# Kernel tuning notes

Measured on AMD Instinct MI355X. Metric: run time of the kernel, lower is better.

## Reference

```python
import jax, jax.numpy as jnp
import numpy as np

B, S, D, H, DK, F = 4, 2048, 1024, 16, 64, 4096


def layer_norm(x, g, b, eps=1e-5):
    mu = jnp.mean(x, axis=-1, keepdims=True)
    var = jnp.var(x, axis=-1, keepdims=True)
    return (x - mu) * jax.lax.rsqrt(var + eps) * g + b


def setup_inputs() -> dict:
    key = jax.random.key(0)
    ks = jax.random.split(key, 16)
    s = 0.02
    return {
        "src": jax.random.normal(ks[0], (B, S, D), jnp.float32),
        # per-head q/k/v projections stacked over heads: (H, D, DK)
        "Wq": jax.random.normal(ks[1], (H, D, DK), jnp.float32) * s,
        "bq": jnp.zeros((H, DK), jnp.float32),
        "Wk": jax.random.normal(ks[2], (H, D, DK), jnp.float32) * s,
        "bk": jnp.zeros((H, DK), jnp.float32),
        "Wv": jax.random.normal(ks[3], (H, D, DK), jnp.float32) * s,
        "bv": jnp.zeros((H, DK), jnp.float32),
        "Wo": jax.random.normal(ks[4], (H * DK, D), jnp.float32) * s,
        "bo": jnp.zeros((D,), jnp.float32),
        "ln1_g": jnp.ones((D,), jnp.float32),
        "ln1_b": jnp.zeros((D,), jnp.float32),
        "W1": jax.random.normal(ks[5], (D, F), jnp.float32) * s,
        "b1": jnp.zeros((F,), jnp.float32),
        "W2": jax.random.normal(ks[6], (F, D), jnp.float32) * s,
        "b2": jnp.zeros((D,), jnp.float32),
        "ln2_g": jnp.ones((D,), jnp.float32),
        "ln2_b": jnp.zeros((D,), jnp.float32),
    }


def reference(src, Wq, bq, Wk, bk, Wv, bv, Wo, bo, ln1_g, ln1_b, W1, b1, W2, b2, ln2_g, ln2_b):
    # --- multi-head attention (all heads batched via einsum) ---
    q = jnp.einsum("bsd,hdk->bhsk", src, Wq) + bq[None, :, None, :]
    k = jnp.einsum("bsd,hdk->bhsk", src, Wk) + bk[None, :, None, :]
    v = jnp.einsum("bsd,hdk->bhsk", src, Wv) + bv[None, :, None, :]
    scale = jnp.sqrt(jnp.asarray(DK, q.dtype))
    scores = jnp.einsum("bhqk,bhsk->bhqs", q, k) / scale  # [B,H,S,S]
    p = jax.nn.softmax(scores, axis=-1)
    ctx = jnp.einsum("bhqs,bhsk->bhqk", p, v)             # [B,H,S,DK]
    ctx = ctx.transpose(0, 2, 1, 3).reshape(src.shape[0], src.shape[1], H * DK)
    attn_out = ctx @ Wo + bo
    x = layer_norm(src + attn_out, ln1_g, ln1_b)
    # --- feed-forward ---
    ff = jax.nn.relu(x @ W1 + b1) @ W2 + b2
    return layer_norm(x + ff, ln2_g, ln2_b)
```

## Files before the change

kernel.cpp:

```cpp
#include <hip/hip_runtime.h>
#include <hip/hip_bf16.h>
#include <cstddef>
#include <cstdint>

typedef __bf16 bf16;
typedef __bf16 bf16x4 __attribute__((ext_vector_type(4)));
typedef __bf16 bf16x8 __attribute__((ext_vector_type(8)));
typedef float f32x4 __attribute__((ext_vector_type(4)));
typedef float f32x16 __attribute__((ext_vector_type(16)));
typedef unsigned int u32x4 __attribute__((ext_vector_type(4)));

#define GLD_LDS16(g, l) __builtin_amdgcn_global_load_lds( \
    (const __attribute__((address_space(1))) void*)(g),   \
    (__attribute__((address_space(3))) void*)(l), 16, 0, 0)

#define SBAR __builtin_amdgcn_s_barrier()
#define SCHED0 __builtin_amdgcn_sched_barrier(0)

static __device__ inline unsigned int cvtpk(float lo, float hi) {
  unsigned int r;
  asm("v_cvt_pk_bf16_f32 %0, %1, %2" : "=v"(r) : "v"(lo), "v"(hi));
  return r;
}
static __device__ inline void plswap(unsigned int& a, unsigned int& b) {
  asm("v_permlane32_swap_b32 %0, %1" : "+v"(a), "+v"(b));
}
static __device__ inline float fexp2(float x) {
#if __has_builtin(__builtin_amdgcn_exp2f)
  return __builtin_amdgcn_exp2f(x);
#else
  float r; asm("v_exp_f32 %0, %1" : "=v"(r) : "v"(x)); return r;
#endif
}
static __device__ inline float tsum16(const float* e) {
  float s0 = e[0] + e[1], s1 = e[2] + e[3], s2 = e[4] + e[5], s3 = e[6] + e[7];
  float s4 = e[8] + e[9], s5 = e[10] + e[11], s6 = e[12] + e[13], s7 = e[14] + e[15];
  return ((s0 + s1) + (s2 + s3)) + ((s4 + s5) + (s6 + s7));
}

__global__ void __launch_bounds__(256)
k_cast(const float* __restrict__ in, bf16* __restrict__ out) {
  int gid = blockIdx.x * 256 + threadIdx.x;
  f32x4 a = ((const f32x4*)in)[gid * 2];
  f32x4 b = ((const f32x4*)in)[gid * 2 + 1];
  bf16x8 o;
#pragma unroll
  for (int i = 0; i < 4; ++i) { o[i] = (bf16)a[i]; o[i + 4] = (bf16)b[i]; }
  ((bf16x8*)out)[gid] = o;
}

__global__ void __launch_bounds__(256)
k_transpose_t(const float* __restrict__ in, bf16* __restrict__ out, int R, int C) {
  __shared__ float tile[64][68];
  const int nct = C >> 6;
  const int bc = blockIdx.x % nct, br = blockIdx.x / nct;
  const int r0 = br << 6, c0 = bc << 6;
  const int t = threadIdx.x;
  const int tr = t >> 4, tc4 = (t & 15) << 2;
#pragma unroll
  for (int i = 0; i < 4; ++i)
    *(f32x4*)&tile[i * 16 + tr][tc4] =
        *(const f32x4*)&in[(size_t)(r0 + i * 16 + tr) * C + c0 + tc4];
  __syncthreads();
  const int c = t >> 2, rch = (t & 3) << 4;
  bf16 ob[16];
#pragma unroll
  for (int j = 0; j < 16; ++j) ob[j] = (bf16)tile[rch + j][c];
  bf16* dst = out + (size_t)(c0 + c) * R + r0 + rch;
  *(bf16x8*)&dst[0] = *(bf16x8*)&ob[0];
  *(bf16x8*)&dst[8] = *(bf16x8*)&ob[8];
}

__global__ void __launch_bounds__(256)
k_reorder_qkv_t(const float* __restrict__ Wq, const float* __restrict__ Wk,
                const float* __restrict__ Wv, bf16* __restrict__ WqkvT) {
  __shared__ float tile[64][68];
  const int bid = blockIdx.x;
  const int sub = bid >> 4, tl = bid & 15;
  const int proj = sub >> 4, h = sub & 15;
  const float* W = (proj == 0) ? Wq : (proj == 1) ? Wk : Wv;
  const float* src = W + (size_t)h * 65536;
  const int r0 = tl << 6;
  const int t = threadIdx.x, tr = t >> 4, tc4 = (t & 15) << 2;
#pragma unroll
  for (int i = 0; i < 4; ++i)
    *(f32x4*)&tile[i * 16 + tr][tc4] =
        *(const f32x4*)&src[(size_t)(r0 + i * 16 + tr) * 64 + tc4];
  __syncthreads();
  const int c = t >> 2, rch = (t & 3) << 4;
  bf16 ob[16];
#pragma unroll
  for (int j = 0; j < 16; ++j) ob[j] = (bf16)tile[rch + j][c];
  bf16* dst = WqkvT + ((size_t)(proj * 1024 + h * 64 + c)) * 1024 + r0 + rch;
  *(bf16x8*)&dst[0] = *(bf16x8*)&ob[0];
  *(bf16x8*)&dst[8] = *(bf16x8*)&ob[8];
}

__global__ void __launch_bounds__(256)
k_bias_qkv(const float* __restrict__ bq, const float* __restrict__ bk,
           const float* __restrict__ bv, float* __restrict__ bqkv) {
  int n = blockIdx.x * 256 + threadIdx.x;
  int proj = n >> 10, wi = n & 1023;
  const float* bb = (proj == 0) ? bq : (proj == 1) ? bk : bv;
  bqkv[n] = bb[wi];
}

template <int MODE, int NREP>
__global__ void __launch_bounds__(512, 1)
k_gemm8(const bf16* __restrict__ A, const bf16* __restrict__ Bt,
        const float* __restrict__ bias, void* __restrict__ outp,
        int M, int N, int K,
        bf16* __restrict__ qb, bf16* __restrict__ kb, bf16* __restrict__ vb) {
  constexpr int BN = 128 * NREP;
  constexpr int BROWS = 64 * NREP;
  __shared__ __align__(16) bf16 Asl[4][8192];
  __shared__ __align__(16) bf16 Bsl[4][BROWS * 64];

  const int tid = threadIdx.x;
  const int lane = tid & 63, wave = tid >> 6;
  const int l16 = lane & 15, lq = lane >> 4;
  const int qwm = wave >> 2, qwn = wave & 3;

  const int mtiles = M >> 8;
  const int nwg = gridDim.x, cpx = nwg >> 3;
  const int wg = (blockIdx.x & 7) * cpx + (blockIdx.x >> 3);
  const int tile_m = (wg % mtiles) << 8;
  const int tile_n = (wg / mtiles) * BN;

  const bf16* Abase = A + (size_t)tile_m * K;
  const bf16* Bbase = Bt + (size_t)tile_n * K;

  const int crow = tid >> 3;
  const int ccol = ((tid & 7) ^ (crow & 7)) << 3;

  auto stageA = [&](int T, int h, int slot) {
    const bf16* s_ = Abase + (size_t)(h * 128 + crow) * K + T * 64 + ccol;
    GLD_LDS16(s_, &Asl[slot][tid * 8]);
    GLD_LDS16(s_ + (size_t)64 * K, &Asl[slot][tid * 8 + 4096]);
  };
  auto stageB = [&](int T, int h, int slot) {
    const bf16* s_ = Bbase + (size_t)(h * BROWS + crow) * K + T * 64 + ccol;
    GLD_LDS16(s_, &Bsl[slot][tid * 8]);
    if (NREP == 2) GLD_LDS16(s_ + (size_t)64 * K, &Bsl[slot][tid * 8 + 4096]);
  };

  const int xk = l16 & 7;
  const int swz0 = (lq ^ xk) * 16;
  const int swz1 = ((4 | lq) ^ xk) * 16;
  const int arow_b = (qwm * 64 + l16) * 128;
  const int brow_b = (qwn * 16 * NREP + l16) * 128;

  bf16x8 af[4][2];
  bf16x8 bb[2][NREP][2];
  f32x4 acc[2][2][4][NREP] = {};

  auto dsA = [&](int slot) {
    const char* Ab = (const char*)&Asl[slot][0] + arow_b;
#pragma unroll
    for (int mi = 0; mi < 4; ++mi) {
      af[mi][0] = *(const bf16x8*)(Ab + mi * 2048 + swz0);
      af[mi][1] = *(const bf16x8*)(Ab + mi * 2048 + swz1);
    }
  };
  auto dsB = [&](int slot, int h) {
    const char* Bb = (const char*)&Bsl[slot][0] + brow_b;
#pragma unroll
    for (int ni = 0; ni < NREP; ++ni) {
      bb[h][ni][0] = *(const bf16x8*)(Bb + ni * 2048 + swz0);
      bb[h][ni][1] = *(const bf16x8*)(Bb + ni * 2048 + swz1);
    }
  };

#define MF(mh, nh)                                                           \
  {                                                                          \
    __builtin_amdgcn_s_setprio(1);                                           \
    _Pragma("unroll") for (int mi = 0; mi < 4; ++mi)                         \
        _Pragma("unroll") for (int ni = 0; ni < NREP; ++ni)                  \
        _Pragma("unroll") for (int p = 0; p < 2; ++p)                        \
            acc[mh][nh][mi][ni] = __builtin_amdgcn_mfma_f32_16x16x32_bf16(   \
                af[mi][p], bb[nh][ni][p], acc[mh][nh][mi][ni], 0, 0, 0);     \
    __builtin_amdgcn_s_setprio(0);                                           \
  }
#define VMW(n) asm volatile("s_waitcnt vmcnt(" #n ")" ::: "memory")

  const int NT = K >> 6;
  const int NI = NT >> 1;

  stageA(0, 0, 0); stageA(0, 1, 1); stageB(0, 0, 0); stageB(0, 1, 1);
  stageA(1, 0, 2); stageB(1, 0, 2); stageB(1, 1, 3);
  SCHED0;
  if (NREP == 2) { VMW(6); } else { VMW(4); }
  SBAR;

  for (int i = 0; i < NI; ++i) {
    const int t2 = 2 * i + 2, t3 = 2 * i + 3;
    const bool tv = (t2 < NT);
    const bool last = (i == NI - 1);
    dsA(0); dsB(0, 0);
    stageA(2 * i + 1, 1, 3);
    SBAR; MF(0, 0); SBAR;
    dsB(1, 1);
    if (tv) stageA(t2, 0, 0);
    SBAR; MF(0, 1); SBAR;
    dsA(1);
    if (tv) stageB(t2, 0, 0);
    SBAR; MF(1, 0); SBAR;
    if (tv) stageB(t2, 1, 1);
    SCHED0;
    if (last) { VMW(0); }
    else if (NREP == 2) { VMW(6); }
    else { VMW(4); }
    SBAR; MF(1, 1); SBAR;
    dsA(2); dsB(2, 0);
    if (tv) stageA(t2, 1, 1);
    SBAR; MF(0, 0); SBAR;
    dsB(3, 1);
    if (tv) stageA(t3, 0, 2);
    SBAR; MF(0, 1); SBAR;
    dsA(3);
    if (tv) stageB(t3, 0, 2);
    SBAR; MF(1, 0); SBAR;
    if (tv) stageB(t3, 1, 3);
    if (!last) {
      SCHED0;
      if (NREP == 2) { VMW(6); } else { VMW(4); }
    }
    SBAR; MF(1, 1); SBAR;
  }
#undef MF
#undef VMW

#pragma unroll
  for (int mh = 0; mh < 2; ++mh)
#pragma unroll
    for (int nh = 0; nh < 2; ++nh)
#pragma unroll
      for (int mi = 0; mi < 4; ++mi)
#pragma unroll
        for (int ni = 0; ni < NREP; ++ni) {
          const int gn = tile_n + nh * (BN / 2) + qwn * 16 * NREP + ni * 16 + l16;
          const float bv = bias[gn];
          f32x4 v = acc[mh][nh][mi][ni];
          const int gm0 = tile_m + mh * 128 + qwm * 64 + mi * 16 + lq * 4;
          if (MODE == 0) {
            int proj = gn >> 10, wi = gn & 1023;
            int h = wi >> 6, dk = wi & 63;
            int b = gm0 >> 11, sdx = gm0 & 2047;
            size_t bhs = (size_t)((b << 4) + h);
            if (proj == 0) {
#pragma unroll
              for (int i2 = 0; i2 < 4; ++i2)
                qb[(bhs * 2048 + sdx + i2) * 64 + dk] = (bf16)((v[i2] + bv) * 0.18033688f);
            } else if (proj == 1) {
#pragma unroll
              for (int i2 = 0; i2 < 4; ++i2)
                kb[(bhs * 2048 + sdx + i2) * 64 + dk] = (bf16)(v[i2] + bv);
            } else {
              bf16x4 pk;
#pragma unroll
              for (int i2 = 0; i2 < 4; ++i2) pk[i2] = (bf16)(v[i2] + bv);
              *(bf16x4*)&vb[(bhs * 64 + dk) * 2048 + sdx] = pk;
            }
          } else if (MODE == 1) {
#pragma unroll
            for (int i2 = 0; i2 < 4; ++i2)
              ((bf16*)outp)[(size_t)(gm0 + i2) * N + gn] = (bf16)(v[i2] + bv);
          } else {
#pragma unroll
            for (int i2 = 0; i2 < 4; ++i2)
              ((bf16*)outp)[(size_t)(gm0 + i2) * N + gn] = (bf16)fmaxf(v[i2] + bv, 0.f);
          }
        }
}

__global__ void __launch_bounds__(256, 2)
k_attn(const bf16* __restrict__ qb, const bf16* __restrict__ kb,
       const bf16* __restrict__ vb, bf16* __restrict__ ctx) {
  __shared__ __align__(16) bf16 KsL[3][4096];
  __shared__ __align__(16) bf16 VsL[3][4096];

  const int bid = blockIdx.x;
  const int wg = (bid & 7) * 64 + (bid >> 3);
  const int bh = wg >> 3, qt = wg & 7;

  const bf16* Qp  = qb + (size_t)bh * 131072 + (size_t)qt * 16384;
  const bf16* Kbh = kb + (size_t)bh * 131072;
  const bf16* Vbh = vb + (size_t)bh * 131072;

  const int tid = threadIdx.x, wave = tid >> 6, lane = tid & 63;
  const int l31 = lane & 31, hi = lane >> 5;

  bf16x8 qfA[4], qfB[4];
  {
    const bf16* qra = Qp + (size_t)(wave * 64 + l31) * 64 + hi * 8;
    const bf16* qrb = qra + 32 * 64;
#pragma unroll
    for (int kd = 0; kd < 4; ++kd) {
      qfA[kd] = *(const bf16x8*)(qra + kd * 16);
      qfB[kd] = *(const bf16x8*)(qrb + kd * 16);
    }
  }

  const int c0 = tid, c1 = tid + 256;
  const int sw0 = ((c0 ^ (c0 >> 3)) & 7) * 8, rw0 = c0 >> 3;
  const int sw1 = ((c1 ^ (c1 >> 3)) & 7) * 8, rw1 = c1 >> 3;
  const int kof0 = rw0 * 64 + sw0, kof1 = rw1 * 64 + sw1;
  const int vof0 = rw0 * 2048 + sw0, vof1 = rw1 * 2048 + sw1;

  const int xr = (hi << 4) ^ ((l31 & 7) << 4);
  const int rb = l31 * 128 + xr;

  f32x16 oA[2] = {}, oB[2] = {};
  float lA = 0.f, lB = 0.f;

#define STAGE_KV(buf, s0)                                             \
  do {                                                                \
    GLD_LDS16(Kbh + (size_t)(s0) * 64 + kof0, &KsL[buf][c0 * 8]);     \
    GLD_LDS16(Kbh + (size_t)(s0) * 64 + kof1, &KsL[buf][c1 * 8]);     \
    GLD_LDS16(Vbh + (s0) + vof0, &VsL[buf][c0 * 8]);                  \
    GLD_LDS16(Vbh + (s0) + vof1, &VsL[buf][c1 * 8]);                  \
  } while (0)

  STAGE_KV(0, 0);
  STAGE_KV(1, 64);

  int cur = 0;
  for (int kt = 0; kt < 32; ++kt) {
    SCHED0;
    if (kt == 31) { asm volatile("s_waitcnt vmcnt(0)" ::: "memory"); }
    else          { asm volatile("s_waitcnt vmcnt(4)" ::: "memory"); }
    __builtin_amdgcn_s_barrier();
    SCHED0;

    if (kt < 30) {
      int nx = cur + 2; if (nx >= 3) nx -= 3;
      STAGE_KV(nx, (kt + 2) * 64);
    }

    const char* Kc = (const char*)&KsL[cur][0];
    const char* Vc = (const char*)&VsL[cur][0];

    bf16x8 paA[4], paB[4];
#pragma unroll
    for (int st = 0; st < 2; ++st) {
      f32x16 sA = {}, sB = {};
      __builtin_amdgcn_s_setprio(1);
#pragma unroll
      for (int kd = 0; kd < 4; ++kd) {
        bf16x8 a = *(const bf16x8*)(Kc + st * 4096 + (rb ^ (kd << 5)));
        sA = __builtin_amdgcn_mfma_f32_32x32x16_bf16(a, qfA[kd], sA, 0, 0, 0);
        sB = __builtin_amdgcn_mfma_f32_32x32x16_bf16(a, qfB[kd], sB, 0, 0, 0);
      }
      __builtin_amdgcn_s_setprio(0);

      float eA[16], eB[16];
#pragma unroll
      for (int i = 0; i < 16; ++i) {
        eA[i] = fexp2(sA[i]);
        eB[i] = fexp2(sB[i]);
      }
      lA += tsum16(eA);
      lB += tsum16(eB);
      unsigned int qdA[4][2], qdB[4][2];
#pragma unroll
      for (int g = 0; g < 4; ++g)
#pragma unroll
        for (int w = 0; w < 2; ++w) {
          qdA[g][w] = cvtpk(eA[g * 4 + w * 2], eA[g * 4 + w * 2 + 1]);
          qdB[g][w] = cvtpk(eB[g * 4 + w * 2], eB[g * 4 + w * 2 + 1]);
        }
#pragma unroll
      for (int a2 = 0; a2 < 2; ++a2) {
        unsigned int x0 = qdA[2 * a2][0], y0 = qdA[2 * a2 + 1][0];
        unsigned int x1 = qdA[2 * a2][1], y1 = qdA[2 * a2 + 1][1];
        plswap(x0, y0); plswap(x1, y1);
        u32x4 fA = {x0, x1, y0, y1};
        paA[st * 2 + a2] = __builtin_bit_cast(bf16x8, fA);
        unsigned int u0 = qdB[2 * a2][0], v0 = qdB[2 * a2 + 1][0];
        unsigned int u1 = qdB[2 * a2][1], v1 = qdB[2 * a2 + 1][1];
        plswap(u0, v0); plswap(u1, v1);
        u32x4 fB = {u0, u1, v0, v1};
        paB[st * 2 + a2] = __builtin_bit_cast(bf16x8, fB);
      }
    }

    __builtin_amdgcn_s_setprio(1);
#pragma unroll
    for (int nd = 0; nd < 2; ++nd)
#pragma unroll
      for (int ks = 0; ks < 4; ++ks) {
        bf16x8 vf = *(const bf16x8*)(Vc + nd * 4096 + (rb ^ (ks << 5)));
        oA[nd] = __builtin_amdgcn_mfma_f32_32x32x16_bf16(paA[ks], vf, oA[nd], 0, 0, 0);
        oB[nd] = __builtin_amdgcn_mfma_f32_32x32x16_bf16(paB[ks], vf, oB[nd], 0, 0, 0);
      }
    __builtin_amdgcn_s_setprio(0);

    if (++cur == 3) cur = 0;
  }
#undef STAGE_KV

  const float ltA = lA + __shfl_xor(lA, 32);
  const float ltB = lB + __shfl_xor(lB, 32);
  const float ivA = 1.f / ltA;
  const float ivB = 1.f / ltB;

  const int b = bh >> 4, h = bh & 15;
  const size_t rowbase = (size_t)(b * 2048 + qt * 256 + wave * 64);
#pragma unroll
  for (int r = 0; r < 16; ++r) {
    const int qr = (r & 3) + 8 * (r >> 2) + 4 * hi;
    const float dA = __shfl(ivA, qr);
    const float dB = __shfl(ivB, qr);
#pragma unroll
    for (int nd = 0; nd < 2; ++nd) {
      const int dk = nd * 32 + l31;
      ctx[(rowbase + qr) * 1024 + h * 64 + dk]      = (bf16)(oA[nd][r] * dA);
      ctx[(rowbase + 32 + qr) * 1024 + h * 64 + dk] = (bf16)(oB[nd][r] * dB);
    }
  }
}

template <typename RT, typename DT, typename OT>
__global__ void __launch_bounds__(256)
k_ln(const RT* __restrict__ resid, const DT* __restrict__ delta,
     const float* __restrict__ g, const float* __restrict__ bta,
     OT* __restrict__ out) {
  const int row = blockIdx.x, tid = threadIdx.x;
  const int wave = tid >> 6, lane = tid & 63;
  __shared__ float rs_[4], rs2_[4];
  const RT* r = resid + (size_t)row * 1024;
  const DT* d = delta + (size_t)row * 1024;
  OT* o = out + (size_t)row * 1024;
  float x[4], s = 0.f, s2 = 0.f;
#pragma unroll
  for (int j = 0; j < 4; ++j) {
    int idx = tid + j * 256;
    float v = (float)r[idx] + (float)d[idx];
    x[j] = v; s += v; s2 += v * v;
  }
#pragma unroll
  for (int m = 32; m >= 1; m >>= 1) { s += __shfl_xor(s, m); s2 += __shfl_xor(s2, m); }
  if (lane == 0) { rs_[wave] = s; rs2_[wave] = s2; }
  __syncthreads();
  float ts = rs_[0] + rs_[1] + rs_[2] + rs_[3];
  float ts2 = rs2_[0] + rs2_[1] + rs2_[2] + rs2_[3];
  float mean = ts * (1.f / 1024.f);
  float var = ts2 * (1.f / 1024.f) - mean * mean;
  float rstd = rsqrtf(var + 1e-5f);
#pragma unroll
  for (int j = 0; j < 4; ++j) {
    int idx = tid + j * 256;
    o[idx] = (OT)((x[j] - mean) * rstd * g[idx] + bta[idx]);
  }
}

extern "C" void kernel_launch(void* const* d_in, const int* in_sizes, int n_in,
                              void* d_out, int out_size, void* d_ws, size_t ws_size,
                              hipStream_t stream) {
  const float* src  = (const float*)d_in[0];
  const float* Wq   = (const float*)d_in[1];
  const float* bq   = (const float*)d_in[2];
  const float* Wk   = (const float*)d_in[3];
  const float* bk   = (const float*)d_in[4];
  const float* Wv   = (const float*)d_in[5];
  const float* bv   = (const float*)d_in[6];
  const float* Wo   = (const float*)d_in[7];
  const float* bo   = (const float*)d_in[8];
  const float* ln1g = (const float*)d_in[9];
  const float* ln1b = (const float*)d_in[10];
  const float* W1   = (const float*)d_in[11];
  const float* b1   = (const float*)d_in[12];
  const float* W2   = (const float*)d_in[13];
  const float* b2   = (const float*)d_in[14];
  const float* ln2g = (const float*)d_in[15];
  const float* ln2b = (const float*)d_in[16];

  char* p = (char*)d_ws;
  bf16*  WqkvT = (bf16*)p;  p += (size_t)3072 * 1024 * 2;
  float* bqkv  = (float*)p; p += 16384;
  bf16*  WoT   = (bf16*)p;  p += (size_t)1024 * 1024 * 2;
  bf16*  W1T   = (bf16*)p;  p += (size_t)4096 * 1024 * 2;
  bf16*  W2T   = (bf16*)p;  p += (size_t)1024 * 4096 * 2;
  bf16*  srcb  = (bf16*)p;  p += (size_t)8388608 * 2;
  bf16*  qbuf  = (bf16*)p;  p += (size_t)8388608 * 2;
  bf16*  kbuf  = (bf16*)p;  p += (size_t)8388608 * 2;
  bf16*  vbuf  = (bf16*)p;  p += (size_t)8388608 * 2;
  bf16*  ctx   = (bf16*)p;  p += (size_t)8388608 * 2;
  bf16*  x1    = (bf16*)p;  p += (size_t)8388608 * 2;
  bf16*  ff1   = (bf16*)p;  p += (size_t)8192 * 4096 * 2;
  bf16*  tmp   = qbuf;

  k_cast<<<4096, 256, 0, stream>>>(src, srcb);
  k_reorder_qkv_t<<<768, 256, 0, stream>>>(Wq, Wk, Wv, WqkvT);
  k_bias_qkv<<<12, 256, 0, stream>>>(bq, bk, bv, bqkv);
  k_transpose_t<<<256, 256, 0, stream>>>(Wo, WoT, 1024, 1024);
  k_transpose_t<<<1024, 256, 0, stream>>>(W1, W1T, 1024, 4096);
  k_transpose_t<<<1024, 256, 0, stream>>>(W2, W2T, 4096, 1024);

  k_gemm8<0, 1><<<768, 512, 0, stream>>>(srcb, WqkvT, bqkv, nullptr,
                                         8192, 3072, 1024, qbuf, kbuf, vbuf);
  k_attn<<<512, 256, 0, stream>>>(qbuf, kbuf, vbuf, ctx);
  k_gemm8<1, 1><<<256, 512, 0, stream>>>(ctx, WoT, bo, tmp,
                                         8192, 1024, 1024, nullptr, nullptr, nullptr);
  k_ln<float, bf16, bf16><<<8192, 256, 0, stream>>>(src, tmp, ln1g, ln1b, x1);
  k_gemm8<2, 2><<<512, 512, 0, stream>>>(x1, W1T, b1, ff1,
                                         8192, 4096, 1024, nullptr, nullptr, nullptr);
  k_gemm8<1, 1><<<256, 512, 0, stream>>>(ff1, W2T, b2, tmp,
                                         8192, 1024, 4096, nullptr, nullptr, nullptr);
  k_ln<bf16, bf16, float><<<8192, 256, 0, stream>>>(x1, tmp, ln2g, ln2b, (float*)d_out);
}
```

Before: 525.2 us.

## Restructure GEMM main loop into four phases and drop XCD block remap

The GEMM main loop now runs four MFMA phases per double K-step instead of eight. Each phase computes both N-halves for one M-half after loading both B slots at once. This halves the barrier count per iteration and regroups the global-to-LDS staging, with new vmcnt wait thresholds. The workgroup index remapping that spread consecutive tiles across the 8 XCDs is removed in favour of the plain blockIdx order, which changes L2 locality. The changes raise register pressure for B fragments, and the hand-tuned wait counts risk races or stalls if they are miscounted.

```diff
diff --git a/kernel.cpp b/kernel.cpp
--- a/kernel.cpp
+++ b/kernel.cpp
@@ -16,6 +16,7 @@
 
 #define SBAR __builtin_amdgcn_s_barrier()
 #define SCHED0 __builtin_amdgcn_sched_barrier(0)
+#define VMW(n) asm volatile("s_waitcnt vmcnt(" #n ")" ::: "memory")
 
 static __device__ inline unsigned int cvtpk(float lo, float hi) {
   unsigned int r;
@@ -107,7 +108,7 @@
 
 template <int MODE, int NREP>
 __global__ void __launch_bounds__(512, 1)
-k_gemm8(const bf16* __restrict__ A, const bf16* __restrict__ Bt,
+k_gemm4(const bf16* __restrict__ A, const bf16* __restrict__ Bt,
         const float* __restrict__ bias, void* __restrict__ outp,
         int M, int N, int K,
         bf16* __restrict__ qb, bf16* __restrict__ kb, bf16* __restrict__ vb) {
@@ -122,8 +123,7 @@
   const int qwm = wave >> 2, qwn = wave & 3;
 
   const int mtiles = M >> 8;
-  const int nwg = gridDim.x, cpx = nwg >> 3;
-  const int wg = (blockIdx.x & 7) * cpx + (blockIdx.x >> 3);
+  const int wg = blockIdx.x;
   const int tile_m = (wg % mtiles) << 8;
   const int tile_n = (wg / mtiles) * BN;
 
@@ -162,26 +162,31 @@
       af[mi][1] = *(const bf16x8*)(Ab + mi * 2048 + swz1);
     }
   };
-  auto dsB = [&](int slot, int h) {
-    const char* Bb = (const char*)&Bsl[slot][0] + brow_b;
+  auto dsB2 = [&](int slot0, int slot1) {
+    const char* B0 = (const char*)&Bsl[slot0][0] + brow_b;
+    const char* B1 = (const char*)&Bsl[slot1][0] + brow_b;
 #pragma unroll
     for (int ni = 0; ni < NREP; ++ni) {
-      bb[h][ni][0] = *(const bf16x8*)(Bb + ni * 2048 + swz0);
-      bb[h][ni][1] = *(const bf16x8*)(Bb + ni * 2048 + swz1);
+      bb[0][ni][0] = *(const bf16x8*)(B0 + ni * 2048 + swz0);
+      bb[0][ni][1] = *(const bf16x8*)(B0 + ni * 2048 + swz1);
+      bb[1][ni][0] = *(const bf16x8*)(B1 + ni * 2048 + swz0);
+      bb[1][ni][1] = *(const bf16x8*)(B1 + ni * 2048 + swz1);
     }
   };
-
-#define MF(mh, nh)                                                           \
-  {                                                                          \
-    __builtin_amdgcn_s_setprio(1);                                           \
-    _Pragma("unroll") for (int mi = 0; mi < 4; ++mi)                         \
-        _Pragma("unroll") for (int ni = 0; ni < NREP; ++ni)                  \
-        _Pragma("unroll") for (int p = 0; p < 2; ++p)                        \
-            acc[mh][nh][mi][ni] = __builtin_amdgcn_mfma_f32_16x16x32_bf16(   \
-                af[mi][p], bb[nh][ni][p], acc[mh][nh][mi][ni], 0, 0, 0);     \
-    __builtin_amdgcn_s_setprio(0);                                           \
-  }
-#define VMW(n) asm volatile("s_waitcnt vmcnt(" #n ")" ::: "memory")
+  auto MF2 = [&](int mh) {
+    __builtin_amdgcn_s_setprio(1);
+#pragma unroll
+    for (int nh = 0; nh < 2; ++nh)
+#pragma unroll
+      for (int mi = 0; mi < 4; ++mi)
+#pragma unroll
+        for (int ni = 0; ni < NREP; ++ni)
+#pragma unroll
+          for (int p = 0; p < 2; ++p)
+            acc[mh][nh][mi][ni] = __builtin_amdgcn_mfma_f32_16x16x32_bf16(
+                af[mi][p], bb[nh][ni][p], acc[mh][nh][mi][ni], 0, 0, 0);
+    __builtin_amdgcn_s_setprio(0);
+  };
 
   const int NT = K >> 6;
   const int NI = NT >> 1;
@@ -195,40 +200,31 @@
   for (int i = 0; i < NI; ++i) {
     const int t2 = 2 * i + 2, t3 = 2 * i + 3;
     const bool tv = (t2 < NT);
-    const bool last = (i == NI - 1);
-    dsA(0); dsB(0, 0);
+    dsA(0); dsB2(0, 1);
     stageA(2 * i + 1, 1, 3);
-    SBAR; MF(0, 0); SBAR;
-    dsB(1, 1);
-    if (tv) stageA(t2, 0, 0);
-    SBAR; MF(0, 1); SBAR;
+    SCHED0;
+    if (NREP == 2) { VMW(10); } else { VMW(7); }
+    SBAR; MF2(0); SBAR;
     dsA(1);
-    if (tv) stageB(t2, 0, 0);
-    SBAR; MF(1, 0); SBAR;
-    if (tv) stageB(t2, 1, 1);
+    if (tv) { stageA(t2, 0, 0); stageB(t2, 0, 0); }
     SCHED0;
-    if (last) { VMW(0); }
-    else if (NREP == 2) { VMW(6); }
-    else { VMW(4); }
-    SBAR; MF(1, 1); SBAR;
-    dsA(2); dsB(2, 0);
-    if (tv) stageA(t2, 1, 1);
-    SBAR; MF(0, 0); SBAR;
-    dsB(3, 1);
-    if (tv) stageA(t3, 0, 2);
-    SBAR; MF(0, 1); SBAR;
+    if (!tv) { VMW(2); }
+    else if (NREP == 2) { VMW(6); } else { VMW(5); }
+    SBAR; MF2(1); SBAR;
+    dsA(2); dsB2(2, 3);
+    if (tv) { stageA(t2, 1, 1); stageB(t2, 1, 1); }
+    SCHED0;
+    if (!tv) { VMW(0); }
+    else if (NREP == 2) { VMW(8); } else { VMW(6); }
+    SBAR; MF2(0); SBAR;
     dsA(3);
-    if (tv) stageB(t3, 0, 2);
-    SBAR; MF(1, 0); SBAR;
-    if (tv) stageB(t3, 1, 3);
-    if (!last) {
+    if (tv) {
+      stageA(t3, 0, 2); stageB(t3, 0, 2); stageB(t3, 1, 3);
       SCHED0;
       if (NREP == 2) { VMW(6); } else { VMW(4); }
     }
-    SBAR; MF(1, 1); SBAR;
+    SBAR; MF2(1); SBAR;
   }
-#undef MF
-#undef VMW
 
 #pragma unroll
   for (int mh = 0; mh < 2; ++mh)
@@ -327,8 +323,8 @@
   int cur = 0;
   for (int kt = 0; kt < 32; ++kt) {
     SCHED0;
-    if (kt == 31) { asm volatile("s_waitcnt vmcnt(0)" ::: "memory"); }
-    else          { asm volatile("s_waitcnt vmcnt(4)" ::: "memory"); }
+    if (kt == 31) { VMW(0); }
+    else          { VMW(4); }
     __builtin_amdgcn_s_barrier();
     SCHED0;
 
@@ -497,15 +493,15 @@
   k_transpose_t<<<1024, 256, 0, stream>>>(W1, W1T, 1024, 4096);
   k_transpose_t<<<1024, 256, 0, stream>>>(W2, W2T, 4096, 1024);
 
-  k_gemm8<0, 1><<<768, 512, 0, stream>>>(srcb, WqkvT, bqkv, nullptr,
+  k_gemm4<0, 1><<<768, 512, 0, stream>>>(srcb, WqkvT, bqkv, nullptr,
                                          8192, 3072, 1024, qbuf, kbuf, vbuf);
   k_attn<<<512, 256, 0, stream>>>(qbuf, kbuf, vbuf, ctx);
-  k_gemm8<1, 1><<<256, 512, 0, stream>>>(ctx, WoT, bo, tmp,
+  k_gemm4<1, 1><<<256, 512, 0, stream>>>(ctx, WoT, bo, tmp,
                                          8192, 1024, 1024, nullptr, nullptr, nullptr);
   k_ln<float, bf16, bf16><<<8192, 256, 0, stream>>>(src, tmp, ln1g, ln1b, x1);
-  k_gemm8<2, 2><<<512, 512, 0, stream>>>(x1, W1T, b1, ff1,
+  k_gemm4<2, 2><<<512, 512, 0, stream>>>(x1, W1T, b1, ff1,
                                          8192, 4096, 1024, nullptr, nullptr, nullptr);
-  k_gemm8<1, 1><<<256, 512, 0, stream>>>(ff1, W2T, b2, tmp,
+  k_gemm4<1, 1><<<256, 512, 0, stream>>>(ff1, W2T, b2, tmp,
                                          8192, 1024, 4096, nullptr, nullptr, nullptr);
   k_ln<bf16, bf16, float><<<8192, 256, 0, stream>>>(x1, tmp, ln2g, ln2b, (float*)d_out);
 }
```

Measured after the change: 493.3 us. 6.1% less time.
